# Performance work log

Measured on AMD Instinct MI355X. Metric: run time of the kernel, lower is better.

The kernel has to match this reference:

```python
import jax, jax.numpy as jnp
import numpy as np

FEATURE_DIM = 4
LOSS_WEIGHT = 1.0
DELTA_V = 0.5
DELTA_D = 1.5
NUM_LABELS = 8  # instance ids 0..7; 0 = background
B, H, W = 16, 640, 640


def _safe_norm(x, axis):
    # L2 norm with grad-safe sqrt (forward value exact: 0 when sum of squares is 0)
    sq = jnp.sum(x * x, axis=axis)
    pos = sq > 0
    return jnp.where(pos, jnp.sqrt(jnp.where(pos, sq, 1.0)), 0.0)


def _single_loss(emb, instance, kernel, training_mask):
    # emb: [H,W,C], instance: [H,W] int, kernel/training_mask: [H,W] float
    C = emb.shape[-1]
    L = NUM_LABELS
    tm = training_mask > 0.5
    kr = kernel > 0.5
    inst = jnp.where(tm, instance, 0).reshape(-1)          # [P]
    inst_k = jnp.where(kr.reshape(-1), inst, 0)            # [P]
    emb_f = emb.reshape(-1, C)                              # [P,C]

    # per-label kernel-region means (emb_mean), label 0 column is zeros
    sums = jax.ops.segment_sum(emb_f, inst_k, num_segments=L)                       # [L,C]
    cnts = jax.ops.segment_sum(jnp.ones(inst_k.shape, jnp.float32), inst_k, L)      # [L]
    mu = sums / jnp.maximum(cnts, 1.0)[:, None]
    mu = mu.at[0].set(0.0)

    # aggregation term: per-pixel distance to its instance mean
    d = _safe_norm(emb_f - mu[inst], axis=1)                                         # [P]
    term = jnp.log(jnp.maximum(d - DELTA_V, 0.0) ** 2 + 1.0)
    cnt_i = jax.ops.segment_sum(jnp.ones(inst.shape, jnp.float32), inst, L)
    agg = jax.ops.segment_sum(term, inst, L) / jnp.maximum(cnt_i, 1.0)               # [L]
    # original skips label 0, then takes mean of l_agg[1:] -> drops first nonzero label
    l_agg = jnp.mean(agg[2:])

    # discrimination term: all ordered pairs of distinct nonzero labels
    dd = _safe_norm(mu[:, None, :] - mu[None, :, :], axis=-1)                        # [L,L]
    valid = (1.0 - jnp.eye(L, dtype=jnp.float32)).at[0, :].set(0.0).at[:, 0].set(0.0)
    dis = jnp.log(jnp.maximum(2.0 * DELTA_D - dd, 0.0) ** 2 + 1.0)
    l_dis = jnp.sum(dis * valid) / jnp.sum(valid)

    l_reg = jnp.mean(jnp.log(_safe_norm(mu, axis=1) + 1.0)) * 0.001
    return l_agg + l_dis + l_reg


def reference(emb, instance, kernel, training_mask):
    losses = jax.vmap(_single_loss)(emb, instance, kernel, training_mask)  # [B]
    return LOSS_WEIGHT * jnp.mean(losses)


def setup_inputs() -> dict:
    key = jax.random.key(0)
    k1, k2, k3 = jax.random.split(key, 3)
    emb = jax.random.normal(k1, (B, H, W, FEATURE_DIM), dtype=jnp.float32)
    instance = jax.random.randint(k2, (B, H, W), 0, NUM_LABELS, dtype=jnp.int32)
    kernel = jax.random.uniform(k3, (B, H, W), dtype=jnp.float32)
    training_mask = jnp.ones((B, H, W), dtype=jnp.float32)
    return {"emb": emb, "instance": instance, "kernel": kernel, "training_mask": training_mask}
```

## Files before the change

kernel.cpp:

```cpp
#include <hip/hip_runtime.h>
#include <math.h>

#define NLAB 8
#define BATCH 16
#define S_OFF  0
#define CK_OFF 28
#define CI_OFF 35
#define AG_OFF 41
#define ACC_PER_B 48
#define ACC_FLOATS (BATCH * ACC_PER_B)
#define LAB_OFFSET 4096
#define GRIDX 200

__device__ __forceinline__ float wave_reduce(float v) {
#pragma unroll
  for (int off = 32; off > 0; off >>= 1) v += __shfl_xor(v, off, 64);
  return v;
}

__global__ __launch_bounds__(256, 4) void k_accum(
    const float4* __restrict__ emb, const int* __restrict__ inst,
    const float* __restrict__ ker, const float* __restrict__ tmk,
    float* __restrict__ acc, unsigned char* __restrict__ labc,
    int P, int use_cache)
{
  const int b = blockIdx.y;
  const size_t base = (size_t)b * P;
  const float4* e  = emb + base;
  const int*    ip = inst + base;
  const float*  kp = ker + base;
  const float*  tp = tmk + base;
  unsigned char* lb = labc + base;

  float s[7][4], ck[7], ci[6];
#pragma unroll
  for (int l = 0; l < 7; ++l) {
    ck[l] = 0.f;
    s[l][0] = 0.f; s[l][1] = 0.f; s[l][2] = 0.f; s[l][3] = 0.f;
  }
#pragma unroll
  for (int l = 0; l < 6; ++l) ci[l] = 0.f;

  const int T   = blockDim.x * gridDim.x;
  const int tid = blockIdx.x * blockDim.x + threadIdx.x;

  for (int p0 = tid; p0 < P; p0 += 4 * T) {
    const int p1 = p0 + T, p2 = p0 + 2 * T, p3 = p0 + 3 * T;
    const bool v1 = p1 < P, v2 = p2 < P, v3 = p3 < P;
    const int q1 = v1 ? p1 : p0, q2 = v2 ? p2 : p0, q3 = v3 ? p3 : p0;

    int   i0 = ip[p0], i1 = ip[q1], i2 = ip[q2], i3 = ip[q3];
    float t0v = tp[p0], t1v = tp[q1], t2v = tp[q2], t3v = tp[q3];
    float c0v = kp[p0], c1v = kp[q1], c2v = kp[q2], c3v = kp[q3];
    float4 e0 = e[p0], e1 = e[q1], e2 = e[q2], e3 = e[q3];

    int lab0 = (t0v > 0.5f)       ? (i0 & 7) : 0;
    int lab1 = (v1 && t1v > 0.5f) ? (i1 & 7) : 0;
    int lab2 = (v2 && t2v > 0.5f) ? (i2 & 7) : 0;
    int lab3 = (v3 && t3v > 0.5f) ? (i3 & 7) : 0;
    float k0 = (c0v > 0.5f) ? 1.f : 0.f;
    float k1 = (c1v > 0.5f) ? 1.f : 0.f;
    float k2 = (c2v > 0.5f) ? 1.f : 0.f;
    float k3 = (c3v > 0.5f) ? 1.f : 0.f;

    if (use_cache) {
      lb[p0] = (unsigned char)lab0;
      if (v1) lb[p1] = (unsigned char)lab1;
      if (v2) lb[p2] = (unsigned char)lab2;
      if (v3) lb[p3] = (unsigned char)lab3;
    }

#pragma unroll
    for (int l = 1; l < NLAB; ++l) {
      float m0 = (lab0 == l) ? 1.f : 0.f;
      float m1 = (lab1 == l) ? 1.f : 0.f;
      float m2 = (lab2 == l) ? 1.f : 0.f;
      float m3 = (lab3 == l) ? 1.f : 0.f;
      float mk0 = m0 * k0, mk1 = m1 * k1, mk2 = m2 * k2, mk3 = m3 * k3;
      ck[l - 1] += (mk0 + mk1) + (mk2 + mk3);
      s[l - 1][0] = fmaf(mk0, e0.x, fmaf(mk1, e1.x, fmaf(mk2, e2.x, fmaf(mk3, e3.x, s[l - 1][0]))));
      s[l - 1][1] = fmaf(mk0, e0.y, fmaf(mk1, e1.y, fmaf(mk2, e2.y, fmaf(mk3, e3.y, s[l - 1][1]))));
      s[l - 1][2] = fmaf(mk0, e0.z, fmaf(mk1, e1.z, fmaf(mk2, e2.z, fmaf(mk3, e3.z, s[l - 1][2]))));
      s[l - 1][3] = fmaf(mk0, e0.w, fmaf(mk1, e1.w, fmaf(mk2, e2.w, fmaf(mk3, e3.w, s[l - 1][3]))));
      if (l >= 2) ci[l - 2] += (m0 + m1) + (m2 + m3);
    }
  }

  __shared__ float red[4][48];
  const int wid = threadIdx.x >> 6, lane = threadIdx.x & 63;
#pragma unroll
  for (int l = 0; l < 7; ++l) {
#pragma unroll
    for (int c = 0; c < 4; ++c) {
      float v = wave_reduce(s[l][c]);
      if (lane == 0) red[wid][S_OFF + l * 4 + c] = v;
    }
    float vk = wave_reduce(ck[l]);
    if (lane == 0) red[wid][CK_OFF + l] = vk;
  }
#pragma unroll
  for (int l = 0; l < 6; ++l) {
    float vi = wave_reduce(ci[l]);
    if (lane == 0) red[wid][CI_OFF + l] = vi;
  }
  __syncthreads();
  if (threadIdx.x < AG_OFF) {
    float v = red[0][threadIdx.x] + red[1][threadIdx.x] +
              red[2][threadIdx.x] + red[3][threadIdx.x];
    atomicAdd(acc + b * ACC_PER_B + threadIdx.x, v);
  }
}

__global__ __launch_bounds__(256, 4) void k_agg(
    const float4* __restrict__ emb, const int* __restrict__ inst,
    const float* __restrict__ tmk, const unsigned char* __restrict__ labc,
    float* __restrict__ acc, int P, int use_cache)
{
  const int b = blockIdx.y;
  const size_t base = (size_t)b * P;
  __shared__ float4 smu[NLAB];
  const float* accB = acc + b * ACC_PER_B;
  if (threadIdx.x < NLAB) {
    int l = threadIdx.x;
    float4 m;
    if (l == 0) {
      m = make_float4(0.f, 0.f, 0.f, 0.f);
    } else {
      float inv = 1.f / fmaxf(accB[CK_OFF + l - 1], 1.f);
      m = make_float4(accB[S_OFF + (l - 1) * 4 + 0] * inv,
                      accB[S_OFF + (l - 1) * 4 + 1] * inv,
                      accB[S_OFF + (l - 1) * 4 + 2] * inv,
                      accB[S_OFF + (l - 1) * 4 + 3] * inv);
    }
    smu[l] = m;
  }
  __syncthreads();

  const float4* e = emb + base;
  const unsigned char* lb = labc + base;
  const int*   ip = inst + base;
  const float* tp = tmk + base;

  float aggl[6];
#pragma unroll
  for (int l = 0; l < 6; ++l) aggl[l] = 0.f;

  const int T   = blockDim.x * gridDim.x;
  const int tid = blockIdx.x * blockDim.x + threadIdx.x;

  for (int p0 = tid; p0 < P; p0 += 4 * T) {
    const int p1 = p0 + T, p2 = p0 + 2 * T, p3 = p0 + 3 * T;
    const bool v1 = p1 < P, v2 = p2 < P, v3 = p3 < P;
    const int q1 = v1 ? p1 : p0, q2 = v2 ? p2 : p0, q3 = v3 ? p3 : p0;

    int lab0, lab1, lab2, lab3;
    if (use_cache) {
      lab0 = lb[p0];
      lab1 = v1 ? lb[p1] : 0;
      lab2 = v2 ? lb[p2] : 0;
      lab3 = v3 ? lb[p3] : 0;
    } else {
      int   i0 = ip[p0], i1 = ip[q1], i2 = ip[q2], i3 = ip[q3];
      float t0v = tp[p0], t1v = tp[q1], t2v = tp[q2], t3v = tp[q3];
      lab0 = (t0v > 0.5f)       ? (i0 & 7) : 0;
      lab1 = (v1 && t1v > 0.5f) ? (i1 & 7) : 0;
      lab2 = (v2 && t2v > 0.5f) ? (i2 & 7) : 0;
      lab3 = (v3 && t3v > 0.5f) ? (i3 & 7) : 0;
    }
    float4 e0 = e[p0], e1 = e[q1], e2 = e[q2], e3 = e[q3];

#pragma unroll
    for (int i = 0; i < 4; ++i) {
      int lab = (i == 0) ? lab0 : (i == 1) ? lab1 : (i == 2) ? lab2 : lab3;
      float4 ev = (i == 0) ? e0 : (i == 1) ? e1 : (i == 2) ? e2 : e3;
      float4 mv = smu[lab];
      float dx = ev.x - mv.x, dy = ev.y - mv.y;
      float dz = ev.z - mv.z, dw = ev.w - mv.w;
      float sq = dx * dx + dy * dy + dz * dz + dw * dw;
      float d = sqrtf(sq);
      float t = fmaxf(d - 0.5f, 0.f);
      float term = (lab >= 2) ? logf(fmaf(t, t, 1.f)) : 0.f;
#pragma unroll
      for (int l = 0; l < 6; ++l) aggl[l] += (lab == l + 2) ? term : 0.f;
    }
  }

  __shared__ float red[4][8];
  const int wid = threadIdx.x >> 6, lane = threadIdx.x & 63;
#pragma unroll
  for (int l = 0; l < 6; ++l) {
    float v = wave_reduce(aggl[l]);
    if (lane == 0) red[wid][l] = v;
  }
  __syncthreads();
  if (threadIdx.x < 6) {
    float v = red[0][threadIdx.x] + red[1][threadIdx.x] +
              red[2][threadIdx.x] + red[3][threadIdx.x];
    atomicAdd(acc + b * ACC_PER_B + AG_OFF + threadIdx.x, v);
  }
}

__global__ void k_final(const float* __restrict__ acc, float* __restrict__ out, int nb) {
  const int lane = threadIdx.x;
  float loss = 0.f;
  if (lane < nb) {
    const float* a = acc + lane * ACC_PER_B;
    float mu[NLAB][4];
#pragma unroll
    for (int c = 0; c < 4; ++c) mu[0][c] = 0.f;
#pragma unroll
    for (int l = 1; l < NLAB; ++l) {
      float inv = 1.f / fmaxf(a[CK_OFF + l - 1], 1.f);
#pragma unroll
      for (int c = 0; c < 4; ++c) mu[l][c] = a[S_OFF + (l - 1) * 4 + c] * inv;
    }
    float l_agg = 0.f;
#pragma unroll
    for (int l = 2; l < NLAB; ++l)
      l_agg += a[AG_OFF + l - 2] / fmaxf(a[CI_OFF + l - 2], 1.f);
    l_agg *= (1.f / 6.f);
    float ssum = 0.f;
    for (int i = 1; i < NLAB; ++i)
      for (int j = 1; j < NLAB; ++j) {
        if (i == j) continue;
        float dx = mu[i][0] - mu[j][0], dy = mu[i][1] - mu[j][1];
        float dz = mu[i][2] - mu[j][2], dw = mu[i][3] - mu[j][3];
        float dd = sqrtf(dx * dx + dy * dy + dz * dz + dw * dw);
        float t = fmaxf(3.0f - dd, 0.f);
        ssum += logf(fmaf(t, t, 1.f));
      }
    float l_dis = ssum / 42.f;
    float rsum = 0.f;
#pragma unroll
    for (int l = 1; l < NLAB; ++l) {
      float n = sqrtf(mu[l][0] * mu[l][0] + mu[l][1] * mu[l][1] +
                      mu[l][2] * mu[l][2] + mu[l][3] * mu[l][3]);
      rsum += logf(n + 1.f);
    }
    float l_reg = rsum * (0.001f / NLAB);
    loss = l_agg + l_dis + l_reg;
  }
  loss = wave_reduce(loss);
  if (lane == 0) out[0] = loss / (float)nb;
}

extern "C" void kernel_launch(void* const* d_in, const int* in_sizes, int n_in,
                              void* d_out, int out_size, void* d_ws, size_t ws_size,
                              hipStream_t stream) {
  const float4* emb = (const float4*)d_in[0];
  const int*    inst = (const int*)d_in[1];
  const float*  ker  = (const float*)d_in[2];
  const float*  tmk  = (const float*)d_in[3];
  float* out = (float*)d_out;

  const int total = in_sizes[1];
  const int P = total / BATCH;

  float* acc = (float*)d_ws;
  unsigned char* labc = (unsigned char*)((char*)d_ws + LAB_OFFSET);
  const size_t need = (size_t)LAB_OFFSET + (size_t)total;
  const int use_cache = (ws_size >= need) ? 1 : 0;

  hipMemsetAsync(d_ws, 0, ACC_FLOATS * sizeof(float), stream);

  dim3 grid(GRIDX, BATCH);
  k_accum<<<grid, 256, 0, stream>>>(emb, inst, ker, tmk, acc, labc, P, use_cache);
  k_agg  <<<grid, 256, 0, stream>>>(emb, inst, tmk, labc, acc, P, use_cache);
  k_final<<<1, 64, 0, stream>>>(acc, out, BATCH);
}
```

Baseline: 246.5 us.

## Fuse accumulate, aggregate and final passes into one cooperative kernel with grid sync

Replaces the three launches with a single cooperative kernel. Each thread keeps its pixels' labels packed in a 64-bit register, so the second pass skips reading instance and mask and skips background pixels. Counts are kept as packed 8-bit lanes, per-label sums go through LDS atomics, and grid-wide syncs separate the phases. This removes the label cache traffic and the launch gaps, at the cost of LDS atomic contention and needing all 2048 blocks to be co-resident. If the cooperative launch fails, it falls back to the old path.

```diff
diff --git a/kernel.cpp b/kernel.cpp
--- a/kernel.cpp
+++ b/kernel.cpp
@@ -1,5 +1,8 @@
 #include <hip/hip_runtime.h>
+#include <hip/hip_cooperative_groups.h>
 #include <math.h>
+
+namespace cg = cooperative_groups;
 
 #define NLAB 8
 #define BATCH 16
@@ -10,12 +13,205 @@
 #define ACC_PER_B 48
 #define ACC_FLOATS (BATCH * ACC_PER_B)
 #define LAB_OFFSET 4096
-#define GRIDX 200
-
-__device__ __forceinline__ float wave_reduce(float v) {
+#define GRIDX 128
+
+typedef unsigned long long ull;
+
+__device__ __forceinline__ float wrf(float v) {
 #pragma unroll
   for (int off = 32; off > 0; off >>= 1) v += __shfl_xor(v, off, 64);
   return v;
+}
+__device__ __forceinline__ ull wr64(ull v) {
+#pragma unroll
+  for (int off = 32; off > 0; off >>= 1) v += __shfl_xor(v, off, 64);
+  return v;
+}
+
+__global__ __launch_bounds__(256, 8) void k_fused(
+    const float4* __restrict__ emb, const int* __restrict__ inst,
+    const float* __restrict__ ker, const float* __restrict__ tmk,
+    float* __restrict__ acc, float* __restrict__ out, int P)
+{
+  cg::grid_group grid = cg::this_grid();
+  const int b = blockIdx.y;
+  const size_t base = (size_t)b * P;
+  const float4* e  = emb + base;
+  const int*    ip = inst + base;
+  const float*  kp = ker + base;
+  const float*  tp = tmk + base;
+
+  __shared__ float  s_lds[NLAB][4];
+  __shared__ float  ck_lds[NLAB];
+  __shared__ float  ci_lds[NLAB];
+  __shared__ float4 smu[NLAB];
+  __shared__ float  agg_lds[NLAB];
+
+  if (threadIdx.x < NLAB * 4) ((float*)s_lds)[threadIdx.x] = 0.f;
+  if (threadIdx.x < NLAB) { ck_lds[threadIdx.x] = 0.f; ci_lds[threadIdx.x] = 0.f; }
+  __syncthreads();
+
+  const int T   = GRIDX * 256;
+  const int tid = blockIdx.x * blockDim.x + threadIdx.x;
+  const int nfull = P / T;
+
+  ull packs = 0, ck64 = 0, ci64 = 0;
+
+#define P1_BODY(p_, j_) do {                                              \
+    float4 ev = e[p_];                                                    \
+    int    iv = ip[p_];                                                   \
+    float  tv = tp[p_];                                                   \
+    float  kv = kp[p_];                                                   \
+    int lab = (tv > 0.5f) ? (iv & 7) : 0;                                 \
+    int kf  = (kv > 0.5f) ? 1 : 0;                                        \
+    packs |= (ull)lab << (4 * (j_));                                      \
+    ci64  += 1ull << (8 * lab);                                           \
+    ck64  += (ull)kf << (8 * lab);                                        \
+    if (kf && lab) {                                                      \
+      atomicAdd(&s_lds[lab][0], ev.x);                                    \
+      atomicAdd(&s_lds[lab][1], ev.y);                                    \
+      atomicAdd(&s_lds[lab][2], ev.z);                                    \
+      atomicAdd(&s_lds[lab][3], ev.w);                                    \
+    }                                                                     \
+  } while (0)
+
+#pragma unroll 4
+  for (int j = 0; j < nfull; ++j) {
+    int p = tid + j * T;
+    P1_BODY(p, j);
+  }
+  for (int j = nfull; ; ++j) {
+    int p = tid + j * T;
+    if (p >= P) break;
+    P1_BODY(p, j);
+  }
+#undef P1_BODY
+
+  {
+    const ull M8 = 0x00FF00FF00FF00FFull;
+    ull ckA = wr64(ck64 & M8);
+    ull ckB = wr64((ck64 >> 8) & M8);
+    ull ciA = wr64(ci64 & M8);
+    ull ciB = wr64((ci64 >> 8) & M8);
+    const int lane = threadIdx.x & 63;
+    if (lane == 0) {
+#pragma unroll
+      for (int f = 0; f < 4; ++f) {
+        atomicAdd(&ck_lds[2 * f],     (float)((ckA >> (16 * f)) & 0xFFFF));
+        atomicAdd(&ck_lds[2 * f + 1], (float)((ckB >> (16 * f)) & 0xFFFF));
+        atomicAdd(&ci_lds[2 * f],     (float)((ciA >> (16 * f)) & 0xFFFF));
+        atomicAdd(&ci_lds[2 * f + 1], (float)((ciB >> (16 * f)) & 0xFFFF));
+      }
+    }
+  }
+  __syncthreads();
+  if (threadIdx.x < AG_OFF) {
+    int t = threadIdx.x;
+    float v;
+    if (t < CK_OFF)      v = s_lds[1 + (t >> 2)][t & 3];
+    else if (t < CI_OFF) v = ck_lds[t - CK_OFF + 1];
+    else                 v = ci_lds[t - CI_OFF + 2];
+    atomicAdd(acc + b * ACC_PER_B + t, v);
+  }
+
+  grid.sync();
+
+  {
+    const float* accB = acc + b * ACC_PER_B;
+    if (threadIdx.x < NLAB) {
+      int l = threadIdx.x;
+      float4 m;
+      if (l == 0) {
+        m = make_float4(0.f, 0.f, 0.f, 0.f);
+      } else {
+        float inv = 1.f / fmaxf(accB[CK_OFF + l - 1], 1.f);
+        m = make_float4(accB[S_OFF + (l - 1) * 4 + 0] * inv,
+                        accB[S_OFF + (l - 1) * 4 + 1] * inv,
+                        accB[S_OFF + (l - 1) * 4 + 2] * inv,
+                        accB[S_OFF + (l - 1) * 4 + 3] * inv);
+      }
+      smu[l] = m;
+      agg_lds[l] = 0.f;
+    }
+  }
+  __syncthreads();
+
+#define P2_BODY(p_, j_) do {                                              \
+    int lab = (int)((packs >> (4 * (j_))) & 7);                           \
+    if (lab >= 2) {                                                       \
+      float4 ev = e[p_];                                                  \
+      float4 mv = smu[lab];                                               \
+      float dx = ev.x - mv.x, dy = ev.y - mv.y;                           \
+      float dz = ev.z - mv.z, dw = ev.w - mv.w;                           \
+      float sq = dx * dx + dy * dy + dz * dz + dw * dw;                   \
+      float d  = sqrtf(sq);                                               \
+      float tt = fmaxf(d - 0.5f, 0.f);                                    \
+      float term = logf(fmaf(tt, tt, 1.f));                               \
+      atomicAdd(&agg_lds[lab], term);                                     \
+    }                                                                     \
+  } while (0)
+
+#pragma unroll 4
+  for (int j = 0; j < nfull; ++j) {
+    int p = tid + j * T;
+    P2_BODY(p, j);
+  }
+  for (int j = nfull; ; ++j) {
+    int p = tid + j * T;
+    if (p >= P) break;
+    P2_BODY(p, j);
+  }
+#undef P2_BODY
+
+  __syncthreads();
+  if (threadIdx.x < 6)
+    atomicAdd(acc + b * ACC_PER_B + AG_OFF + threadIdx.x, agg_lds[threadIdx.x + 2]);
+
+  grid.sync();
+
+  if (blockIdx.x == 0 && blockIdx.y == 0 && threadIdx.x < 64) {
+    const int lane = threadIdx.x;
+    float loss = 0.f;
+    if (lane < BATCH) {
+      const float* a = acc + lane * ACC_PER_B;
+      float mu[NLAB][4];
+#pragma unroll
+      for (int c = 0; c < 4; ++c) mu[0][c] = 0.f;
+#pragma unroll
+      for (int l = 1; l < NLAB; ++l) {
+        float inv = 1.f / fmaxf(a[CK_OFF + l - 1], 1.f);
+#pragma unroll
+        for (int c = 0; c < 4; ++c) mu[l][c] = a[S_OFF + (l - 1) * 4 + c] * inv;
+      }
+      float l_agg = 0.f;
+#pragma unroll
+      for (int l = 2; l < NLAB; ++l)
+        l_agg += a[AG_OFF + l - 2] / fmaxf(a[CI_OFF + l - 2], 1.f);
+      l_agg *= (1.f / 6.f);
+      float ssum = 0.f;
+      for (int i = 1; i < NLAB; ++i)
+        for (int j = 1; j < NLAB; ++j) {
+          if (i == j) continue;
+          float dx = mu[i][0] - mu[j][0], dy = mu[i][1] - mu[j][1];
+          float dz = mu[i][2] - mu[j][2], dw = mu[i][3] - mu[j][3];
+          float dd = sqrtf(dx * dx + dy * dy + dz * dz + dw * dw);
+          float t = fmaxf(3.0f - dd, 0.f);
+          ssum += logf(fmaf(t, t, 1.f));
+        }
+      float l_dis = ssum / 42.f;
+      float rsum = 0.f;
+#pragma unroll
+      for (int l = 1; l < NLAB; ++l) {
+        float n = sqrtf(mu[l][0] * mu[l][0] + mu[l][1] * mu[l][1] +
+                        mu[l][2] * mu[l][2] + mu[l][3] * mu[l][3]);
+        rsum += logf(n + 1.f);
+      }
+      float l_reg = rsum * (0.001f / NLAB);
+      loss = l_agg + l_dis + l_reg;
+    }
+    loss = wrf(loss);
+    if (lane == 0) out[0] = loss / (float)BATCH;
+  }
 }
 
 __global__ __launch_bounds__(256, 4) void k_accum(
@@ -92,15 +288,15 @@
   for (int l = 0; l < 7; ++l) {
 #pragma unroll
     for (int c = 0; c < 4; ++c) {
-      float v = wave_reduce(s[l][c]);
+      float v = wrf(s[l][c]);
       if (lane == 0) red[wid][S_OFF + l * 4 + c] = v;
     }
-    float vk = wave_reduce(ck[l]);
+    float vk = wrf(ck[l]);
     if (lane == 0) red[wid][CK_OFF + l] = vk;
   }
 #pragma unroll
   for (int l = 0; l < 6; ++l) {
-    float vi = wave_reduce(ci[l]);
+    float vi = wrf(ci[l]);
     if (lane == 0) red[wid][CI_OFF + l] = vi;
   }
   __syncthreads();
@@ -189,7 +385,7 @@
   const int wid = threadIdx.x >> 6, lane = threadIdx.x & 63;
 #pragma unroll
   for (int l = 0; l < 6; ++l) {
-    float v = wave_reduce(aggl[l]);
+    float v = wrf(aggl[l]);
     if (lane == 0) red[wid][l] = v;
   }
   __syncthreads();
@@ -240,7 +436,7 @@
     float l_reg = rsum * (0.001f / NLAB);
     loss = l_agg + l_dis + l_reg;
   }
-  loss = wave_reduce(loss);
+  loss = wrf(loss);
   if (lane == 0) out[0] = loss / (float)nb;
 }
 
@@ -254,17 +450,27 @@
   float* out = (float*)d_out;
 
   const int total = in_sizes[1];
-  const int P = total / BATCH;
+  int P = total / BATCH;
 
   float* acc = (float*)d_ws;
-  unsigned char* labc = (unsigned char*)((char*)d_ws + LAB_OFFSET);
-  const size_t need = (size_t)LAB_OFFSET + (size_t)total;
-  const int use_cache = (ws_size >= need) ? 1 : 0;
 
   hipMemsetAsync(d_ws, 0, ACC_FLOATS * sizeof(float), stream);
 
-  dim3 grid(GRIDX, BATCH);
-  k_accum<<<grid, 256, 0, stream>>>(emb, inst, ker, tmk, acc, labc, P, use_cache);
-  k_agg  <<<grid, 256, 0, stream>>>(emb, inst, tmk, labc, acc, P, use_cache);
-  k_final<<<1, 64, 0, stream>>>(acc, out, BATCH);
-}
+  const int T = GRIDX * 256;
+  hipError_t cerr = hipErrorUnknown;
+  if (P <= 16 * T) {
+    void* args[] = {(void*)&emb, (void*)&inst, (void*)&ker, (void*)&tmk,
+                    (void*)&acc, (void*)&out, (void*)&P};
+    cerr = hipLaunchCooperativeKernel((void*)k_fused, dim3(GRIDX, BATCH),
+                                      dim3(256), args, 0, stream);
+  }
+  if (cerr != hipSuccess) {
+    unsigned char* labc = (unsigned char*)((char*)d_ws + LAB_OFFSET);
+    const size_t need = (size_t)LAB_OFFSET + (size_t)total;
+    const int use_cache = (ws_size >= need) ? 1 : 0;
+    dim3 grid(200, BATCH);
+    k_accum<<<grid, 256, 0, stream>>>(emb, inst, ker, tmk, acc, labc, P, use_cache);
+    k_agg  <<<grid, 256, 0, stream>>>(emb, inst, tmk, labc, acc, P, use_cache);
+    k_final<<<1, 64, 0, stream>>>(acc, out, BATCH);
+  }
+}
```

New measurement: 738.1 us. +199.4%, slower.

## Raise per-thread ILP to 8, use packed v2 FMAs, and shrink grids

Applied to the files above, without the earlier changes.

Both streaming kernels now issue eight independent loads per thread before computing, with a scheduling barrier so all loads stay ahead of the compute. This is meant to expose more memory-level parallelism. The accumulation kernel packs its sums and counts into 2-wide float vectors so the compiler can emit packed FMA/add instructions, which cuts ALU work. Grid sizes shrink from 200 blocks per image to 64 and 96, and the aggregation kernel's occupancy hint rises to 6. The costs are higher register pressure and possibly too few waves to saturate memory bandwidth.

```diff
diff --git a/kernel.cpp b/kernel.cpp
--- a/kernel.cpp
+++ b/kernel.cpp
@@ -10,7 +10,19 @@
 #define ACC_PER_B 48
 #define ACC_FLOATS (BATCH * ACC_PER_B)
 #define LAB_OFFSET 4096
-#define GRIDX 200
+#define GX_ACC 64
+#define GX_AGG 96
+#define ILP 8
+
+typedef __attribute__((ext_vector_type(2))) float v2f;
+
+__device__ __forceinline__ v2f v2fma(v2f a, v2f b, v2f c) {
+#if defined(__has_builtin) && __has_builtin(__builtin_elementwise_fma)
+  return __builtin_elementwise_fma(a, b, c);
+#else
+  v2f r; r.x = fmaf(a.x, b.x, c.x); r.y = fmaf(a.y, b.y, c.y); return r;
+#endif
+}
 
 __device__ __forceinline__ float wave_reduce(float v) {
 #pragma unroll
@@ -32,76 +44,96 @@
   const float*  tp = tmk + base;
   unsigned char* lb = labc + base;
 
-  float s[7][4], ck[7], ci[6];
-#pragma unroll
-  for (int l = 0; l < 7; ++l) {
-    ck[l] = 0.f;
-    s[l][0] = 0.f; s[l][1] = 0.f; s[l][2] = 0.f; s[l][3] = 0.f;
-  }
-#pragma unroll
-  for (int l = 0; l < 6; ++l) ci[l] = 0.f;
+  v2f s2[7][2], cnt2[7];
+#pragma unroll
+  for (int j = 0; j < 7; ++j) {
+    s2[j][0] = (v2f)(0.f);
+    s2[j][1] = (v2f)(0.f);
+    cnt2[j]  = (v2f)(0.f);
+  }
 
   const int T   = blockDim.x * gridDim.x;
   const int tid = blockIdx.x * blockDim.x + threadIdx.x;
 
-  for (int p0 = tid; p0 < P; p0 += 4 * T) {
-    const int p1 = p0 + T, p2 = p0 + 2 * T, p3 = p0 + 3 * T;
-    const bool v1 = p1 < P, v2 = p2 < P, v3 = p3 < P;
-    const int q1 = v1 ? p1 : p0, q2 = v2 ? p2 : p0, q3 = v3 ? p3 : p0;
-
-    int   i0 = ip[p0], i1 = ip[q1], i2 = ip[q2], i3 = ip[q3];
-    float t0v = tp[p0], t1v = tp[q1], t2v = tp[q2], t3v = tp[q3];
-    float c0v = kp[p0], c1v = kp[q1], c2v = kp[q2], c3v = kp[q3];
-    float4 e0 = e[p0], e1 = e[q1], e2 = e[q2], e3 = e[q3];
-
-    int lab0 = (t0v > 0.5f)       ? (i0 & 7) : 0;
-    int lab1 = (v1 && t1v > 0.5f) ? (i1 & 7) : 0;
-    int lab2 = (v2 && t2v > 0.5f) ? (i2 & 7) : 0;
-    int lab3 = (v3 && t3v > 0.5f) ? (i3 & 7) : 0;
-    float k0 = (c0v > 0.5f) ? 1.f : 0.f;
-    float k1 = (c1v > 0.5f) ? 1.f : 0.f;
-    float k2 = (c2v > 0.5f) ? 1.f : 0.f;
-    float k3 = (c3v > 0.5f) ? 1.f : 0.f;
-
-    if (use_cache) {
-      lb[p0] = (unsigned char)lab0;
-      if (v1) lb[p1] = (unsigned char)lab1;
-      if (v2) lb[p2] = (unsigned char)lab2;
-      if (v3) lb[p3] = (unsigned char)lab3;
+  int p0 = tid;
+  for (; p0 + (ILP - 1) * T < P; p0 += ILP * T) {
+    int   iv[ILP]; float tv[ILP], kv[ILP]; float4 ev[ILP];
+#pragma unroll
+    for (int k = 0; k < ILP; ++k) iv[k] = ip[p0 + k * T];
+#pragma unroll
+    for (int k = 0; k < ILP; ++k) tv[k] = tp[p0 + k * T];
+#pragma unroll
+    for (int k = 0; k < ILP; ++k) kv[k] = kp[p0 + k * T];
+#pragma unroll
+    for (int k = 0; k < ILP; ++k) ev[k] = e[p0 + k * T];
+    __builtin_amdgcn_sched_barrier(0);
+
+    int lab[ILP]; float kf[ILP];
+#pragma unroll
+    for (int k = 0; k < ILP; ++k) {
+      lab[k] = (tv[k] > 0.5f) ? (iv[k] & 7) : 0;
+      kf[k]  = (kv[k] > 0.5f) ? 1.f : 0.f;
+      if (use_cache) lb[p0 + k * T] = (unsigned char)lab[k];
     }
 
 #pragma unroll
     for (int l = 1; l < NLAB; ++l) {
-      float m0 = (lab0 == l) ? 1.f : 0.f;
-      float m1 = (lab1 == l) ? 1.f : 0.f;
-      float m2 = (lab2 == l) ? 1.f : 0.f;
-      float m3 = (lab3 == l) ? 1.f : 0.f;
-      float mk0 = m0 * k0, mk1 = m1 * k1, mk2 = m2 * k2, mk3 = m3 * k3;
-      ck[l - 1] += (mk0 + mk1) + (mk2 + mk3);
-      s[l - 1][0] = fmaf(mk0, e0.x, fmaf(mk1, e1.x, fmaf(mk2, e2.x, fmaf(mk3, e3.x, s[l - 1][0]))));
-      s[l - 1][1] = fmaf(mk0, e0.y, fmaf(mk1, e1.y, fmaf(mk2, e2.y, fmaf(mk3, e3.y, s[l - 1][1]))));
-      s[l - 1][2] = fmaf(mk0, e0.z, fmaf(mk1, e1.z, fmaf(mk2, e2.z, fmaf(mk3, e3.z, s[l - 1][2]))));
-      s[l - 1][3] = fmaf(mk0, e0.w, fmaf(mk1, e1.w, fmaf(mk2, e2.w, fmaf(mk3, e3.w, s[l - 1][3]))));
-      if (l >= 2) ci[l - 2] += (m0 + m1) + (m2 + m3);
+#pragma unroll
+      for (int k = 0; k < ILP; ++k) {
+        float m  = (lab[k] == l) ? 1.f : 0.f;
+        float mk = m * kf[k];
+        v2f mk2; mk2.x = mk; mk2.y = mk;
+        v2f e01; e01.x = ev[k].x; e01.y = ev[k].y;
+        v2f e23; e23.x = ev[k].z; e23.y = ev[k].w;
+        v2f cm;  cm.x = mk; cm.y = m;
+        s2[l - 1][0] = v2fma(mk2, e01, s2[l - 1][0]);
+        s2[l - 1][1] = v2fma(mk2, e23, s2[l - 1][1]);
+        cnt2[l - 1] += cm;
+      }
+    }
+  }
+  for (int p = p0; p < P; p += T) {
+    int   iv = ip[p];
+    float tv = tp[p];
+    float kv = kp[p];
+    float4 ev = e[p];
+    int lab = (tv > 0.5f) ? (iv & 7) : 0;
+    float kf = (kv > 0.5f) ? 1.f : 0.f;
+    if (use_cache) lb[p] = (unsigned char)lab;
+#pragma unroll
+    for (int l = 1; l < NLAB; ++l) {
+      float m  = (lab == l) ? 1.f : 0.f;
+      float mk = m * kf;
+      v2f mk2; mk2.x = mk; mk2.y = mk;
+      v2f e01; e01.x = ev.x; e01.y = ev.y;
+      v2f e23; e23.x = ev.z; e23.y = ev.w;
+      v2f cm;  cm.x = mk; cm.y = m;
+      s2[l - 1][0] = v2fma(mk2, e01, s2[l - 1][0]);
+      s2[l - 1][1] = v2fma(mk2, e23, s2[l - 1][1]);
+      cnt2[l - 1] += cm;
     }
   }
 
   __shared__ float red[4][48];
   const int wid = threadIdx.x >> 6, lane = threadIdx.x & 63;
 #pragma unroll
-  for (int l = 0; l < 7; ++l) {
-#pragma unroll
-    for (int c = 0; c < 4; ++c) {
-      float v = wave_reduce(s[l][c]);
-      if (lane == 0) red[wid][S_OFF + l * 4 + c] = v;
-    }
-    float vk = wave_reduce(ck[l]);
-    if (lane == 0) red[wid][CK_OFF + l] = vk;
-  }
-#pragma unroll
-  for (int l = 0; l < 6; ++l) {
-    float vi = wave_reduce(ci[l]);
-    if (lane == 0) red[wid][CI_OFF + l] = vi;
+  for (int j = 0; j < 7; ++j) {
+    float v0 = wave_reduce(s2[j][0].x);
+    float v1 = wave_reduce(s2[j][0].y);
+    float v2 = wave_reduce(s2[j][1].x);
+    float v3 = wave_reduce(s2[j][1].y);
+    float vk = wave_reduce(cnt2[j].x);
+    if (lane == 0) {
+      red[wid][S_OFF + j * 4 + 0] = v0;
+      red[wid][S_OFF + j * 4 + 1] = v1;
+      red[wid][S_OFF + j * 4 + 2] = v2;
+      red[wid][S_OFF + j * 4 + 3] = v3;
+      red[wid][CK_OFF + j] = vk;
+    }
+    if (j >= 1) {
+      float vi = wave_reduce(cnt2[j].y);
+      if (lane == 0) red[wid][CI_OFF + (j - 1)] = vi;
+    }
   }
   __syncthreads();
   if (threadIdx.x < AG_OFF) {
@@ -111,7 +143,7 @@
   }
 }
 
-__global__ __launch_bounds__(256, 4) void k_agg(
+__global__ __launch_bounds__(256, 6) void k_agg(
     const float4* __restrict__ emb, const int* __restrict__ inst,
     const float* __restrict__ tmk, const unsigned char* __restrict__ labc,
     float* __restrict__ acc, int P, int use_cache)
@@ -148,41 +180,51 @@
   const int T   = blockDim.x * gridDim.x;
   const int tid = blockIdx.x * blockDim.x + threadIdx.x;
 
-  for (int p0 = tid; p0 < P; p0 += 4 * T) {
-    const int p1 = p0 + T, p2 = p0 + 2 * T, p3 = p0 + 3 * T;
-    const bool v1 = p1 < P, v2 = p2 < P, v3 = p3 < P;
-    const int q1 = v1 ? p1 : p0, q2 = v2 ? p2 : p0, q3 = v3 ? p3 : p0;
-
-    int lab0, lab1, lab2, lab3;
+  int p0 = tid;
+  for (; p0 + (ILP - 1) * T < P; p0 += ILP * T) {
+    int lab[ILP]; float4 ev[ILP];
     if (use_cache) {
-      lab0 = lb[p0];
-      lab1 = v1 ? lb[p1] : 0;
-      lab2 = v2 ? lb[p2] : 0;
-      lab3 = v3 ? lb[p3] : 0;
+#pragma unroll
+      for (int k = 0; k < ILP; ++k) lab[k] = lb[p0 + k * T];
     } else {
-      int   i0 = ip[p0], i1 = ip[q1], i2 = ip[q2], i3 = ip[q3];
-      float t0v = tp[p0], t1v = tp[q1], t2v = tp[q2], t3v = tp[q3];
-      lab0 = (t0v > 0.5f)       ? (i0 & 7) : 0;
-      lab1 = (v1 && t1v > 0.5f) ? (i1 & 7) : 0;
-      lab2 = (v2 && t2v > 0.5f) ? (i2 & 7) : 0;
-      lab3 = (v3 && t3v > 0.5f) ? (i3 & 7) : 0;
-    }
-    float4 e0 = e[p0], e1 = e[q1], e2 = e[q2], e3 = e[q3];
-
-#pragma unroll
-    for (int i = 0; i < 4; ++i) {
-      int lab = (i == 0) ? lab0 : (i == 1) ? lab1 : (i == 2) ? lab2 : lab3;
-      float4 ev = (i == 0) ? e0 : (i == 1) ? e1 : (i == 2) ? e2 : e3;
-      float4 mv = smu[lab];
-      float dx = ev.x - mv.x, dy = ev.y - mv.y;
-      float dz = ev.z - mv.z, dw = ev.w - mv.w;
+      int iv[ILP]; float tv[ILP];
+#pragma unroll
+      for (int k = 0; k < ILP; ++k) iv[k] = ip[p0 + k * T];
+#pragma unroll
+      for (int k = 0; k < ILP; ++k) tv[k] = tp[p0 + k * T];
+#pragma unroll
+      for (int k = 0; k < ILP; ++k) lab[k] = (tv[k] > 0.5f) ? (iv[k] & 7) : 0;
+    }
+#pragma unroll
+    for (int k = 0; k < ILP; ++k) ev[k] = e[p0 + k * T];
+    __builtin_amdgcn_sched_barrier(0);
+
+#pragma unroll
+    for (int k = 0; k < ILP; ++k) {
+      float4 mv = smu[lab[k]];
+      float dx = ev[k].x - mv.x, dy = ev[k].y - mv.y;
+      float dz = ev[k].z - mv.z, dw = ev[k].w - mv.w;
       float sq = dx * dx + dy * dy + dz * dz + dw * dw;
-      float d = sqrtf(sq);
-      float t = fmaxf(d - 0.5f, 0.f);
-      float term = (lab >= 2) ? logf(fmaf(t, t, 1.f)) : 0.f;
-#pragma unroll
-      for (int l = 0; l < 6; ++l) aggl[l] += (lab == l + 2) ? term : 0.f;
-    }
+      float d  = sqrtf(sq);
+      float t  = fmaxf(d - 0.5f, 0.f);
+      float term = (lab[k] >= 2) ? logf(fmaf(t, t, 1.f)) : 0.f;
+#pragma unroll
+      for (int l = 0; l < 6; ++l) aggl[l] += (lab[k] == l + 2) ? term : 0.f;
+    }
+  }
+  for (int p = p0; p < P; p += T) {
+    int lab;
+    if (use_cache) lab = lb[p];
+    else           lab = (tp[p] > 0.5f) ? (ip[p] & 7) : 0;
+    float4 ev = e[p];
+    float4 mv = smu[lab];
+    float dx = ev.x - mv.x, dy = ev.y - mv.y;
+    float dz = ev.z - mv.z, dw = ev.w - mv.w;
+    float d = sqrtf(dx * dx + dy * dy + dz * dz + dw * dw);
+    float t = fmaxf(d - 0.5f, 0.f);
+    float term = (lab >= 2) ? logf(fmaf(t, t, 1.f)) : 0.f;
+#pragma unroll
+    for (int l = 0; l < 6; ++l) aggl[l] += (lab == l + 2) ? term : 0.f;
   }
 
   __shared__ float red[4][8];
@@ -263,8 +305,7 @@
 
   hipMemsetAsync(d_ws, 0, ACC_FLOATS * sizeof(float), stream);
 
-  dim3 grid(GRIDX, BATCH);
-  k_accum<<<grid, 256, 0, stream>>>(emb, inst, ker, tmk, acc, labc, P, use_cache);
-  k_agg  <<<grid, 256, 0, stream>>>(emb, inst, tmk, labc, acc, P, use_cache);
+  k_accum<<<dim3(GX_ACC, BATCH), 256, 0, stream>>>(emb, inst, ker, tmk, acc, labc, P, use_cache);
+  k_agg  <<<dim3(GX_AGG, BATCH), 256, 0, stream>>>(emb, inst, tmk, labc, acc, P, use_cache);
   k_final<<<1, 64, 0, stream>>>(acc, out, BATCH);
 }
```

Result: faster. 241.6 us (-2.0%).
